# Kernel optimization log

Hardware: AMD Instinct MI355X
Metric: run time of the kernel (lower is better)

Reference implementation:

```python
import jax, jax.numpy as jnp
import numpy as np

B, L, D, F = 8, 1024, 256, 11
TEMP = D ** 0.5
LN_EPS = 1e-6


def setup_inputs() -> dict:
    key = jax.random.key(0)
    ks = jax.random.split(key, 14)
    mk = lambda k, s: jax.random.normal(k, s, dtype=jnp.float32)
    return {
        "q": mk(ks[0], (B, L, D)),
        "k": mk(ks[1], (B, L, D)),
        "v": mk(ks[2], (B, L, D)),
        "x": jax.random.uniform(ks[3], (B, L, F), dtype=jnp.float32),
        "inputs_lengths": jax.random.randint(ks[4], (B,), 512, L + 1),
        "w_qs": mk(ks[5], (D, D)) * 0.05,
        "w_ks": mk(ks[6], (D, D)) * 0.05,
        "w_vs": mk(ks[7], (D, D)) * 0.05,
        "w_qs2": mk(ks[8], (D, D)) * 0.05,
        "w_ks2": mk(ks[9], (D, D)) * 0.05,
        "w_fc": mk(ks[10], (D, D)) * 0.05,
        "feature_importance": mk(ks[11], (F,)) * 0.1,
        "ln_gamma": jnp.ones((D,), jnp.float32),
        "ln_beta": jnp.zeros((D,), jnp.float32),
    }


def reference(q, k, v, x, w_qs, w_ks, w_vs, w_qs2, w_ks2, w_fc,
              feature_importance, ln_gamma, ln_beta, inputs_lengths):
    lin = lambda a, w: jnp.einsum('bli,oi->blo', a, w)  # torch Linear: y = x W^T
    qp = lin(q, w_qs)
    kp = lin(k, w_ks)
    vp = lin(v, w_vs)
    q2 = lin(q, w_qs2)
    k2 = lin(k, w_ks2)

    # key-position validity mask [B, L]
    key_mask = jnp.arange(L)[None, :] < inputs_lengths[:, None]

    # FeatureSim: pairwise L1 feature distances weighted by feature_importance
    fd = jnp.abs(x[:, :, None, :] - x[:, None, :, :])           # [B,L,L,F]
    fa = jnp.einsum('bijf,f->bij', fd, feature_importance)      # [B,L,L]
    fa = jnp.where(key_mask[:, None, :], fa, -jnp.inf)          # pad_masking
    fa = jax.nn.softmax(fa, axis=-1)
    fa = jnp.nan_to_num(fa)                                     # nan -> 0 for fully-masked rows

    # dual-score attention with tanh activation (no row normalization)
    attn = jnp.einsum('bid,bjd->bij', qp / TEMP, kp)
    q2f = jnp.einsum('bij,bjd->bid', fa, q2)
    k2f = jnp.einsum('bij,bjd->bid', fa, k2)
    attn = attn + jnp.einsum('bid,bjd->bij', q2f / TEMP, k2f)
    zm = key_mask[:, None, :]
    attn = jnp.where(zm, attn, 0.0)                             # pad_zero_masking
    attn = jnp.tanh(attn)
    attn = jnp.where(zm, attn, 0.0)                             # pad_zero_masking (tanh(0)=0, kept for fidelity)

    out = jnp.einsum('bij,bjd->bid', attn, vp)
    out = lin(out, w_fc) + q                                    # dropout is identity at eval
    mu = jnp.mean(out, axis=-1, keepdims=True)
    var = jnp.var(out, axis=-1, keepdims=True)
    out = (out - mu) / jnp.sqrt(var + LN_EPS) * ln_gamma + ln_beta
    return (out, attn)
```

## Files before the change

kernel.cpp:

```cpp
#include <hip/hip_runtime.h>
#include <hip/hip_bf16.h>
#include <math.h>

typedef __hip_bfloat16 bf16;
typedef __bf16 bf16x8 __attribute__((ext_vector_type(8)));
typedef float  f32x4  __attribute__((ext_vector_type(4)));

#define NB 8
#define SL 1024
#define DD 256
#define NF 11
#define RPB 8

#define AS_G __attribute__((address_space(1)))
#define AS_L __attribute__((address_space(3)))

__device__ __forceinline__ bf16x8 ldfrag(const bf16* p) {
  return *reinterpret_cast<const bf16x8*>(p);
}
__device__ __forceinline__ bf16x8 ldfrag(const float* p) {
  const float4 a = *reinterpret_cast<const float4*>(p);
  const float4 b = *reinterpret_cast<const float4*>(p + 4);
  bf16x8 r;
  r[0] = (__bf16)a.x; r[1] = (__bf16)a.y; r[2] = (__bf16)a.z; r[3] = (__bf16)a.w;
  r[4] = (__bf16)b.x; r[5] = (__bf16)b.y; r[6] = (__bf16)b.z; r[7] = (__bf16)b.w;
  return r;
}
__device__ __forceinline__ unsigned short us(float f) {
  bf16 h = __float2bfloat16(f);
  return *reinterpret_cast<unsigned short*>(&h);
}

template<int R>
__device__ __forceinline__ void stage_t(const float* __restrict__ g, int ld,
                                        bf16* __restrict__ s, int tid) {
#pragma unroll
  for (int it = 0; it < R / 32; ++it) {
    const int cid = it * 256 + tid;
    const int row = cid >> 3, c16 = cid & 7;
    bf16x8 v = ldfrag(g + (size_t)row * ld + c16 * 8);
    *reinterpret_cast<bf16x8*>(s + row * 64 + ((c16 ^ (row & 7)) << 3)) = v;
  }
}
template<int R>
__device__ __forceinline__ void stage_t(const bf16* __restrict__ g, int ld,
                                        bf16* __restrict__ s, int tid) {
  const int wbase = tid & ~63;
#pragma unroll
  for (int it = 0; it < R / 32; ++it) {
    const int cid = it * 256 + tid;
    const int row = cid >> 3, sc = cid & 7;
    const int c16 = sc ^ (row & 7);
    const bf16* src = g + (size_t)row * ld + c16 * 8;
    bf16* dst = s + (size_t)(it * 256 + wbase) * 8;
    __builtin_amdgcn_global_load_lds((const AS_G void*)src, (AS_L void*)dst, 16, 0, 0);
  }
}

__device__ __forceinline__ void compute_64x128(const bf16* __restrict__ sA,
                                               const bf16* __restrict__ sB,
                                               int lane, int wave, f32x4 acc[4][2]) {
  const int n15 = lane & 15, quad = lane >> 4;
  const int wn = wave * 32;
#pragma unroll
  for (int kc = 0; kc < 2; ++kc) {
    const int c16 = kc * 4 + quad;
    bf16x8 aF[4], bF[2];
#pragma unroll
    for (int t = 0; t < 4; ++t) {
      const int ra = t * 16 + n15;
      aF[t] = *reinterpret_cast<const bf16x8*>(sA + ra * 64 + ((c16 ^ (ra & 7)) << 3));
    }
#pragma unroll
    for (int t = 0; t < 2; ++t) {
      const int rb = wn + t * 16 + n15;
      bF[t] = *reinterpret_cast<const bf16x8*>(sB + rb * 64 + ((c16 ^ (rb & 7)) << 3));
    }
#pragma unroll
    for (int ti = 0; ti < 4; ++ti)
#pragma unroll
      for (int tj = 0; tj < 2; ++tj)
        acc[ti][tj] = __builtin_amdgcn_mfma_f32_16x16x32_bf16(aF[ti], bF[tj], acc[ti][tj], 0, 0, 0);
  }
}

template<typename TA, typename TB>
__device__ __forceinline__ void gemm_64x128(const TA* __restrict__ A, int lda,
                                            const TB* __restrict__ B, int ldb, int K,
                                            bf16* s, int tid, f32x4 acc[4][2]) {
  const int lane = tid & 63, wave = tid >> 6;
  bf16* sA = s;
  bf16* sB = s + 4096;
  for (int k0 = 0; k0 < K; k0 += 64) {
    stage_t<64>(A + k0, lda, sA, tid);
    stage_t<128>(B + k0, ldb, sB, tid);
    __syncthreads();
    compute_64x128(sA, sB, lane, wave, acc);
    __syncthreads();
  }
}

__device__ __forceinline__ float wred_sum(float v) {
#pragma unroll
  for (int o = 32; o > 0; o >>= 1) v += __shfl_xor(v, o, 64);
  return v;
}

__global__ __launch_bounds__(256) void k_wc(const float* __restrict__ wfc,
                                            const float* __restrict__ wvs,
                                            float* __restrict__ Wc)
{
  const int o = blockIdx.x, m = threadIdx.x;
  const float* fr = wfc + (size_t)o * DD;
  float acc = 0.f;
#pragma unroll 8
  for (int i = 0; i < DD; ++i)
    acc += fr[i] * wvs[(size_t)i * DD + m];
  Wc[(size_t)o * DD + m] = acc;
}

__global__ __launch_bounds__(256) void k_proj(
    const float* __restrict__ q, const float* __restrict__ k, const float* __restrict__ v,
    const float* __restrict__ wqs, const float* __restrict__ wks, const float* __restrict__ Wc,
    const float* __restrict__ wqs2, const float* __restrict__ wks2,
    bf16* __restrict__ qq, bf16* __restrict__ kk,
    bf16* __restrict__ vpwt, bf16* __restrict__ q2t, bf16* __restrict__ k2t)
{
  __shared__ bf16 smem[12288];
  const int tid = threadIdx.x, lane = tid & 63, wave = tid >> 6;
  const int z = blockIdx.z;
  const float* A = (z == 2) ? v : ((z == 1 || z == 4) ? k : q);
  const float* W = (z == 0) ? wqs : (z == 1) ? wks : (z == 2) ? Wc : (z == 3) ? wqs2 : wks2;
  const int rowBase = blockIdx.x * 64;
  const int colBase = blockIdx.y * 128;
  f32x4 acc[4][2] = {};
  gemm_64x128(A + (size_t)rowBase * DD, DD, W + (size_t)colBase * DD, DD, DD, smem, tid, acc);
  const int n15 = lane & 15, quad = lane >> 4;
  const int wn = wave * 32;
  if (z <= 1) {
    bf16* O = (z == 0) ? qq : kk;
#pragma unroll
    for (int ti = 0; ti < 4; ++ti)
#pragma unroll
      for (int tj = 0; tj < 2; ++tj)
#pragma unroll
        for (int r = 0; r < 4; ++r) {
          int row = rowBase + ti * 16 + quad * 4 + r;
          int col = colBase + wn + tj * 16 + n15;
          O[(size_t)row * 512 + col] = __float2bfloat16(acc[ti][tj][r]);
        }
  } else {
    bf16* O = (z == 2) ? vpwt : (z == 3) ? q2t : k2t;
    const int bb = rowBase >> 10, rowInB = rowBase & 1023;
#pragma unroll
    for (int ti = 0; ti < 4; ++ti)
#pragma unroll
      for (int tj = 0; tj < 2; ++tj) {
        int l0  = rowInB + ti * 16 + quad * 4;
        int col = colBase + wn + tj * 16 + n15;
        ushort4 pk = make_ushort4(us(acc[ti][tj][0]), us(acc[ti][tj][1]),
                                  us(acc[ti][tj][2]), us(acc[ti][tj][3]));
        *reinterpret_cast<ushort4*>(&O[((size_t)bb * DD + col) * SL + l0]) = pk;
      }
  }
}

__global__ __launch_bounds__(256) void k_fa(const float* __restrict__ x,
                                            const float* __restrict__ fi_g,
                                            const int* __restrict__ lens,
                                            bf16* __restrict__ fa)
{
  __shared__ __align__(16) float sx[SL * NF];
  __shared__ float sredS[4][RPB];
  const int tid = threadIdx.x, wave = tid >> 6;
  const int b  = blockIdx.x >> 7;
  const int i0 = (blockIdx.x & 127) * RPB;
  {
    const float4* src = reinterpret_cast<const float4*>(x + (size_t)b * SL * NF);
    float4* dst = reinterpret_cast<float4*>(sx);
#pragma unroll
    for (int it = 0; it < 11; ++it) dst[it * 256 + tid] = src[it * 256 + tid];
  }
  float fiv[NF];
#pragma unroll
  for (int f = 0; f < NF; ++f) fiv[f] = fi_g[f];
  const int len = lens[b];
  __syncthreads();
  float xi[RPB][NF];
#pragma unroll
  for (int i = 0; i < RPB; ++i)
#pragma unroll
    for (int f = 0; f < NF; ++f) xi[i][f] = sx[(i0 + i) * NF + f];
  float e[RPB][4];
  float ps[RPB];
#pragma unroll
  for (int i = 0; i < RPB; ++i) ps[i] = 0.f;
#pragma unroll
  for (int t = 0; t < 4; ++t) {
    const int j = tid + t * 256;
    const bool valid = (t < 2) || (j < len);
    float xj[NF];
#pragma unroll
    for (int f = 0; f < NF; ++f) xj[f] = sx[j * NF + f];
#pragma unroll
    for (int i = 0; i < RPB; ++i) {
      float a = 0.f;
#pragma unroll
      for (int f = 0; f < NF; ++f) a += fabsf(xi[i][f] - xj[f]) * fiv[f];
      float ev = valid ? __expf(a) : 0.f;
      e[i][t] = ev;
      ps[i] += ev;
    }
  }
#pragma unroll
  for (int i = 0; i < RPB; ++i) {
    float wsv = wred_sum(ps[i]);
    if ((tid & 63) == 0) sredS[wave][i] = wsv;
  }
  __syncthreads();
  bf16* out = fa + (size_t)b * SL * SL + (size_t)i0 * SL;
#pragma unroll
  for (int i = 0; i < RPB; ++i) {
    const float inv = 1.f / (sredS[0][i] + sredS[1][i] + sredS[2][i] + sredS[3][i]);
#pragma unroll
    for (int t = 0; t < 4; ++t)
      out[(size_t)i * SL + tid + t * 256] = __float2bfloat16(e[i][t] * inv);
  }
}

__global__ __launch_bounds__(256) void k_famul(const bf16* __restrict__ fa,
                                               const bf16* __restrict__ q2t,
                                               const bf16* __restrict__ k2t,
                                               bf16* __restrict__ qq,
                                               bf16* __restrict__ kk)
{
  __shared__ bf16 smem[12288];
  const int tid = threadIdx.x, lane = tid & 63, wave = tid >> 6;
  const int flat = blockIdx.x + 16 * blockIdx.y + 32 * blockIdx.z;
  const int lid  = (flat & 7) * 64 + (flat >> 3);
  const int bx = lid & 15, by = (lid >> 4) & 1, bz = lid >> 5;
  const int b = bz >> 1, which = bz & 1;
  const int iBase = bx * 64, dBase = by * 128;
  const bf16* A  = fa + (size_t)b * SL * SL + (size_t)iBase * SL;
  const bf16* Bm = (which ? k2t : q2t) + (size_t)b * DD * SL + (size_t)dBase * SL;
  f32x4 acc[4][2] = {};
  gemm_64x128(A, SL, Bm, SL, SL, smem, tid, acc);
  bf16* O = (which ? kk : qq) + (size_t)b * SL * 512 + 256;
  const int n15 = lane & 15, quad = lane >> 4;
  const int wn = wave * 32;
#pragma unroll
  for (int ti = 0; ti < 4; ++ti)
#pragma unroll
    for (int tj = 0; tj < 2; ++tj)
#pragma unroll
      for (int r = 0; r < 4; ++r)
        O[(size_t)(iBase + ti * 16 + quad * 4 + r) * 512 +
          dBase + wn + tj * 16 + n15] = __float2bfloat16(acc[ti][tj][r]);
}

__global__ __launch_bounds__(256) void k_attn(const bf16* __restrict__ qq,
                                              const bf16* __restrict__ kk,
                                              const int* __restrict__ lens,
                                              float* __restrict__ attn_f32,
                                              bf16* __restrict__ attn_b16)
{
  __shared__ bf16 smem[12288];
  const int tid = threadIdx.x, lane = tid & 63, wave = tid >> 6;
  const int flat = blockIdx.x + 16 * blockIdx.y + 128 * blockIdx.z;
  const int lid  = (flat & 7) * 128 + (flat >> 3);
  const int bx = lid & 15, by = (lid >> 4) & 7, bz = lid >> 7;
  const int b = bz;
  const int iBase = bx * 64, jBase = by * 128;
  f32x4 acc[4][2] = {};
  gemm_64x128(qq + ((size_t)b * SL + iBase) * 512, 512,
              kk + ((size_t)b * SL + jBase) * 512, 512, 512, smem, tid, acc);
  const int len = lens[b];
  const int n15 = lane & 15, quad = lane >> 4;
  const int wn = wave * 32;
#pragma unroll
  for (int ti = 0; ti < 4; ++ti)
#pragma unroll
    for (int tj = 0; tj < 2; ++tj)
#pragma unroll
      for (int r = 0; r < 4; ++r) {
        int i = iBase + ti * 16 + quad * 4 + r;
        int j = jBase + wn + tj * 16 + n15;
        float vv = (j < len) ? tanhf(acc[ti][tj][r] * (1.f / 16.f)) : 0.f;
        size_t idx = (size_t)b * SL * SL + (size_t)i * SL + j;
        attn_f32[idx] = vv;
        attn_b16[idx] = __float2bfloat16(vv);
      }
}

__global__ __launch_bounds__(256) void k_av(const bf16* __restrict__ attn,
                                            const bf16* __restrict__ vpwt,
                                            const float* __restrict__ qres,
                                            float* __restrict__ fcout)
{
  __shared__ bf16 smem[12288];
  const int tid = threadIdx.x, lane = tid & 63, wave = tid >> 6;
  const int flat = blockIdx.x + 16 * blockIdx.y + 32 * blockIdx.z;
  const int lid  = (flat & 7) * 32 + (flat >> 3);
  const int bx = lid & 15, by = (lid >> 4) & 1, bz = lid >> 5;
  const int b = bz;
  const int iBase = bx * 64, dBase = by * 128;
  f32x4 acc[4][2] = {};
  gemm_64x128(attn + (size_t)b * SL * SL + (size_t)iBase * SL, SL,
              vpwt + (size_t)b * DD * SL + (size_t)dBase * SL, SL, SL, smem, tid, acc);
  const int n15 = lane & 15, quad = lane >> 4;
  const int wn = wave * 32;
#pragma unroll
  for (int ti = 0; ti < 4; ++ti)
#pragma unroll
    for (int tj = 0; tj < 2; ++tj)
#pragma unroll
      for (int r = 0; r < 4; ++r) {
        size_t row = (size_t)b * SL + iBase + ti * 16 + quad * 4 + r;
        int col = dBase + wn + tj * 16 + n15;
        fcout[row * DD + col] = acc[ti][tj][r] + qres[row * DD + col];
      }
}

__global__ __launch_bounds__(256) void k_ln(const float* __restrict__ fcout,
                                            const float* __restrict__ gam,
                                            const float* __restrict__ bet,
                                            float* __restrict__ outp)
{
  __shared__ float r1[4], r2[4];
  const int r = blockIdx.x, tid = threadIdx.x;
  const float v = fcout[(size_t)r * DD + tid];
  float s = wred_sum(v), ss = wred_sum(v * v);
  if ((tid & 63) == 0) { r1[tid >> 6] = s; r2[tid >> 6] = ss; }
  __syncthreads();
  s  = r1[0] + r1[1] + r1[2] + r1[3];
  ss = r2[0] + r2[1] + r2[2] + r2[3];
  const float mean = s * (1.f / DD);
  const float var  = ss * (1.f / DD) - mean * mean;
  float y = (v - mean) * rsqrtf(var + 1e-6f);
  y = y * gam[tid] + bet[tid];
  outp[(size_t)r * DD + tid] = y;
}

extern "C" void kernel_launch(void* const* d_in, const int* in_sizes, int n_in,
                              void* d_out, int out_size, void* d_ws, size_t ws_size,
                              hipStream_t stream)
{
  const float* q    = (const float*)d_in[0];
  const float* k    = (const float*)d_in[1];
  const float* v    = (const float*)d_in[2];
  const float* x    = (const float*)d_in[3];
  const int*  lens  = (const int*)d_in[4];
  const float* wqs  = (const float*)d_in[5];
  const float* wks  = (const float*)d_in[6];
  const float* wvs  = (const float*)d_in[7];
  const float* wqs2 = (const float*)d_in[8];
  const float* wks2 = (const float*)d_in[9];
  const float* wfc  = (const float*)d_in[10];
  const float* fi   = (const float*)d_in[11];
  const float* gam  = (const float*)d_in[12];
  const float* bet  = (const float*)d_in[13];

  char* w = (char*)d_ws;
  const size_t MB = 1u << 20;
  bf16* qq    = (bf16*)(w + 0 * MB);
  bf16* kk    = (bf16*)(w + 8 * MB);
  bf16* vpwt  = (bf16*)(w + 16 * MB);
  bf16* q2t   = (bf16*)(w + 20 * MB);
  bf16* k2t   = (bf16*)(w + 24 * MB);
  bf16* fa    = (bf16*)(w + 28 * MB);
  bf16* attn_b16 = fa;
  float* Wc   = (float*)(w + 28 * MB);
  float* fcout = (float*)(w + 0 * MB);

  float* outp  = (float*)d_out;
  float* attnp = outp + (size_t)NB * SL * DD;

  dim3 blk(256);
  hipLaunchKernelGGL(k_wc,    dim3(256),       blk, 0, stream, wfc, wvs, Wc);
  hipLaunchKernelGGL(k_proj,  dim3(128, 2, 5), blk, 0, stream,
                     q, k, v, wqs, wks, Wc, wqs2, wks2, qq, kk, vpwt, q2t, k2t);
  hipLaunchKernelGGL(k_fa,    dim3(NB * 128),  blk, 0, stream, x, fi, lens, fa);
  hipLaunchKernelGGL(k_famul, dim3(16, 2, 16), blk, 0, stream, fa, q2t, k2t, qq, kk);
  hipLaunchKernelGGL(k_attn,  dim3(16, 8, 8),  blk, 0, stream,
                     qq, kk, lens, attnp, attn_b16);
  hipLaunchKernelGGL(k_av,    dim3(16, 2, 8),  blk, 0, stream, attn_b16, vpwt, q, fcout);
  hipLaunchKernelGGL(k_ln,    dim3(NB * SL),   blk, 0, stream, fcout, gam, bet, outp);
}
```

Before: 208.8 us.

## Share A-tile across paired weight GEMMs in proj and famul, use fast tanh

k_proj now computes the q/q2 and k/k2 projections in one block that stages the shared input tile once and runs two MFMA accumulators against two weight tiles. k_famul likewise computes fa@q2 and fa@k2 together, so the large fa tile is read and staged once instead of twice. The aim is to halve A-operand global and LDS traffic for these GEMMs. The cost is halved grid sizes, which lowers parallelism, plus more LDS and registers per block. Separately, tanhf in k_attn is replaced by an exp-based formula that is cheaper but slightly less accurate.

New measurement: 218.4 us. 4.6% more time.

```diff
diff --git a/kernel.cpp b/kernel.cpp
--- a/kernel.cpp
+++ b/kernel.cpp
@@ -30,6 +30,9 @@
   bf16 h = __float2bfloat16(f);
   return *reinterpret_cast<unsigned short*>(&h);
 }
+__device__ __forceinline__ float tanh_fast(float x) {
+  return 1.f - 2.f / (__expf(2.f * x) + 1.f);
+}
 
 template<int R>
 __device__ __forceinline__ void stage_t(const float* __restrict__ g, int ld,
@@ -81,6 +84,39 @@
 #pragma unroll
       for (int tj = 0; tj < 2; ++tj)
         acc[ti][tj] = __builtin_amdgcn_mfma_f32_16x16x32_bf16(aF[ti], bF[tj], acc[ti][tj], 0, 0, 0);
+  }
+}
+
+__device__ __forceinline__ void compute_64x128x2(const bf16* __restrict__ sA,
+                                                 const bf16* __restrict__ sB1,
+                                                 const bf16* __restrict__ sB2,
+                                                 int lane, int wave,
+                                                 f32x4 acc1[4][2], f32x4 acc2[4][2]) {
+  const int n15 = lane & 15, quad = lane >> 4;
+  const int wn = wave * 32;
+#pragma unroll
+  for (int kc = 0; kc < 2; ++kc) {
+    const int c16 = kc * 4 + quad;
+    bf16x8 aF[4], b1F[2], b2F[2];
+#pragma unroll
+    for (int t = 0; t < 4; ++t) {
+      const int ra = t * 16 + n15;
+      aF[t] = *reinterpret_cast<const bf16x8*>(sA + ra * 64 + ((c16 ^ (ra & 7)) << 3));
+    }
+#pragma unroll
+    for (int t = 0; t < 2; ++t) {
+      const int rb = wn + t * 16 + n15;
+      const int off = rb * 64 + ((c16 ^ (rb & 7)) << 3);
+      b1F[t] = *reinterpret_cast<const bf16x8*>(sB1 + off);
+      b2F[t] = *reinterpret_cast<const bf16x8*>(sB2 + off);
+    }
+#pragma unroll
+    for (int ti = 0; ti < 4; ++ti)
+#pragma unroll
+      for (int tj = 0; tj < 2; ++tj) {
+        acc1[ti][tj] = __builtin_amdgcn_mfma_f32_16x16x32_bf16(aF[ti], b1F[tj], acc1[ti][tj], 0, 0, 0);
+        acc2[ti][tj] = __builtin_amdgcn_mfma_f32_16x16x32_bf16(aF[ti], b2F[tj], acc2[ti][tj], 0, 0, 0);
+      }
   }
 }
 
@@ -126,19 +162,36 @@
     bf16* __restrict__ qq, bf16* __restrict__ kk,
     bf16* __restrict__ vpwt, bf16* __restrict__ q2t, bf16* __restrict__ k2t)
 {
-  __shared__ bf16 smem[12288];
+  __shared__ bf16 smem[20480];
   const int tid = threadIdx.x, lane = tid & 63, wave = tid >> 6;
   const int z = blockIdx.z;
-  const float* A = (z == 2) ? v : ((z == 1 || z == 4) ? k : q);
-  const float* W = (z == 0) ? wqs : (z == 1) ? wks : (z == 2) ? Wc : (z == 3) ? wqs2 : wks2;
+  const float* A  = (z == 0) ? q : (z == 1) ? k : v;
+  const float* W1 = (z == 0) ? wqs : (z == 1) ? wks : Wc;
+  const float* W2 = (z == 0) ? wqs2 : wks2;
+  const bool dual = (z < 2);
   const int rowBase = blockIdx.x * 64;
   const int colBase = blockIdx.y * 128;
-  f32x4 acc[4][2] = {};
-  gemm_64x128(A + (size_t)rowBase * DD, DD, W + (size_t)colBase * DD, DD, DD, smem, tid, acc);
-  const int n15 = lane & 15, quad = lane >> 4;
-  const int wn = wave * 32;
-  if (z <= 1) {
-    bf16* O = (z == 0) ? qq : kk;
+  bf16* sA = smem;
+  bf16* sB1 = smem + 4096;
+  bf16* sB2 = smem + 12288;
+  f32x4 acc1[4][2] = {}, acc2[4][2] = {};
+  const float* Ap  = A  + (size_t)rowBase * DD;
+  const float* B1p = W1 + (size_t)colBase * DD;
+  const float* B2p = W2 + (size_t)colBase * DD;
+  for (int k0 = 0; k0 < DD; k0 += 64) {
+    stage_t<64>(Ap + k0, DD, sA, tid);
+    stage_t<128>(B1p + k0, DD, sB1, tid);
+    if (dual) stage_t<128>(B2p + k0, DD, sB2, tid);
+    __syncthreads();
+    if (dual) compute_64x128x2(sA, sB1, sB2, lane, wave, acc1, acc2);
+    else      compute_64x128(sA, sB1, lane, wave, acc1);
+    __syncthreads();
+  }
+  const int n15 = lane & 15, quad = lane >> 4;
+  const int wn = wave * 32;
+  const int bb = rowBase >> 10, rowInB = rowBase & 1023;
+  if (dual) {
+    bf16* O1 = (z == 0) ? qq : kk;
 #pragma unroll
     for (int ti = 0; ti < 4; ++ti)
 #pragma unroll
@@ -147,20 +200,29 @@
         for (int r = 0; r < 4; ++r) {
           int row = rowBase + ti * 16 + quad * 4 + r;
           int col = colBase + wn + tj * 16 + n15;
-          O[(size_t)row * 512 + col] = __float2bfloat16(acc[ti][tj][r]);
+          O1[(size_t)row * 512 + col] = __float2bfloat16(acc1[ti][tj][r]);
         }
-  } else {
-    bf16* O = (z == 2) ? vpwt : (z == 3) ? q2t : k2t;
-    const int bb = rowBase >> 10, rowInB = rowBase & 1023;
+    bf16* O2 = (z == 0) ? q2t : k2t;
 #pragma unroll
     for (int ti = 0; ti < 4; ++ti)
 #pragma unroll
       for (int tj = 0; tj < 2; ++tj) {
         int l0  = rowInB + ti * 16 + quad * 4;
         int col = colBase + wn + tj * 16 + n15;
-        ushort4 pk = make_ushort4(us(acc[ti][tj][0]), us(acc[ti][tj][1]),
-                                  us(acc[ti][tj][2]), us(acc[ti][tj][3]));
-        *reinterpret_cast<ushort4*>(&O[((size_t)bb * DD + col) * SL + l0]) = pk;
+        ushort4 pk = make_ushort4(us(acc2[ti][tj][0]), us(acc2[ti][tj][1]),
+                                  us(acc2[ti][tj][2]), us(acc2[ti][tj][3]));
+        *reinterpret_cast<ushort4*>(&O2[((size_t)bb * DD + col) * SL + l0]) = pk;
+      }
+  } else {
+#pragma unroll
+    for (int ti = 0; ti < 4; ++ti)
+#pragma unroll
+      for (int tj = 0; tj < 2; ++tj) {
+        int l0  = rowInB + ti * 16 + quad * 4;
+        int col = colBase + wn + tj * 16 + n15;
+        ushort4 pk = make_ushort4(us(acc1[ti][tj][0]), us(acc1[ti][tj][1]),
+                                  us(acc1[ti][tj][2]), us(acc1[ti][tj][3]));
+        *reinterpret_cast<ushort4*>(&vpwt[((size_t)bb * DD + col) * SL + l0]) = pk;
       }
   }
 }
@@ -234,28 +296,43 @@
                                                bf16* __restrict__ qq,
                                                bf16* __restrict__ kk)
 {
-  __shared__ bf16 smem[12288];
+  __shared__ bf16 smem[20480];
   const int tid = threadIdx.x, lane = tid & 63, wave = tid >> 6;
   const int flat = blockIdx.x + 16 * blockIdx.y + 32 * blockIdx.z;
-  const int lid  = (flat & 7) * 64 + (flat >> 3);
+  const int lid  = (flat & 7) * 32 + (flat >> 3);
   const int bx = lid & 15, by = (lid >> 4) & 1, bz = lid >> 5;
-  const int b = bz >> 1, which = bz & 1;
+  const int b = bz;
   const int iBase = bx * 64, dBase = by * 128;
-  const bf16* A  = fa + (size_t)b * SL * SL + (size_t)iBase * SL;
-  const bf16* Bm = (which ? k2t : q2t) + (size_t)b * DD * SL + (size_t)dBase * SL;
-  f32x4 acc[4][2] = {};
-  gemm_64x128(A, SL, Bm, SL, SL, smem, tid, acc);
-  bf16* O = (which ? kk : qq) + (size_t)b * SL * 512 + 256;
-  const int n15 = lane & 15, quad = lane >> 4;
-  const int wn = wave * 32;
+  const bf16* A  = fa  + (size_t)b * SL * SL + (size_t)iBase * SL;
+  const bf16* B1 = q2t + (size_t)b * DD * SL + (size_t)dBase * SL;
+  const bf16* B2 = k2t + (size_t)b * DD * SL + (size_t)dBase * SL;
+  bf16* sA = smem;
+  bf16* sB1 = smem + 4096;
+  bf16* sB2 = smem + 12288;
+  f32x4 acc1[4][2] = {}, acc2[4][2] = {};
+  for (int k0 = 0; k0 < SL; k0 += 64) {
+    stage_t<64>(A + k0, SL, sA, tid);
+    stage_t<128>(B1 + k0, SL, sB1, tid);
+    stage_t<128>(B2 + k0, SL, sB2, tid);
+    __syncthreads();
+    compute_64x128x2(sA, sB1, sB2, lane, wave, acc1, acc2);
+    __syncthreads();
+  }
+  const int n15 = lane & 15, quad = lane >> 4;
+  const int wn = wave * 32;
+  bf16* O1 = qq + (size_t)b * SL * 512 + 256;
+  bf16* O2 = kk + (size_t)b * SL * 512 + 256;
 #pragma unroll
   for (int ti = 0; ti < 4; ++ti)
 #pragma unroll
     for (int tj = 0; tj < 2; ++tj)
 #pragma unroll
-      for (int r = 0; r < 4; ++r)
-        O[(size_t)(iBase + ti * 16 + quad * 4 + r) * 512 +
-          dBase + wn + tj * 16 + n15] = __float2bfloat16(acc[ti][tj][r]);
+      for (int r = 0; r < 4; ++r) {
+        size_t off = (size_t)(iBase + ti * 16 + quad * 4 + r) * 512 +
+                     dBase + wn + tj * 16 + n15;
+        O1[off] = __float2bfloat16(acc1[ti][tj][r]);
+        O2[off] = __float2bfloat16(acc2[ti][tj][r]);
+      }
 }
 
 __global__ __launch_bounds__(256) void k_attn(const bf16* __restrict__ qq,
@@ -285,7 +362,7 @@
       for (int r = 0; r < 4; ++r) {
         int i = iBase + ti * 16 + quad * 4 + r;
         int j = jBase + wn + tj * 16 + n15;
-        float vv = (j < len) ? tanhf(acc[ti][tj][r] * (1.f / 16.f)) : 0.f;
+        float vv = (j < len) ? tanh_fast(acc[ti][tj][r] * (1.f / 16.f)) : 0.f;
         size_t idx = (size_t)b * SL * SL + (size_t)i * SL + j;
         attn_f32[idx] = vv;
         attn_b16[idx] = __float2bfloat16(vv);
@@ -377,10 +454,10 @@
 
   dim3 blk(256);
   hipLaunchKernelGGL(k_wc,    dim3(256),       blk, 0, stream, wfc, wvs, Wc);
-  hipLaunchKernelGGL(k_proj,  dim3(128, 2, 5), blk, 0, stream,
+  hipLaunchKernelGGL(k_proj,  dim3(128, 2, 3), blk, 0, stream,
                      q, k, v, wqs, wks, Wc, wqs2, wks2, qq, kk, vpwt, q2t, k2t);
   hipLaunchKernelGGL(k_fa,    dim3(NB * 128),  blk, 0, stream, x, fi, lens, fa);
-  hipLaunchKernelGGL(k_famul, dim3(16, 2, 16), blk, 0, stream, fa, q2t, k2t, qq, kk);
+  hipLaunchKernelGGL(k_famul, dim3(16, 2, 8),  blk, 0, stream, fa, q2t, k2t, qq, kk);
   hipLaunchKernelGGL(k_attn,  dim3(16, 8, 8),  blk, 0, stream,
                      qq, kk, lens, attnp, attn_b16);
   hipLaunchKernelGGL(k_av,    dim3(16, 2, 8),  blk, 0, stream, attn_b16, vpwt, q, fcout);
```
